# Kernel tuning notes

Measured on AMD Instinct MI355X. Metric: run time of the kernel, lower is better.

The kernel has to match this reference:

```python
import jax, jax.numpy as jnp
import numpy as np

MU = 0            # smeared direction (init arg dir)
IS_ODD = False    # init arg is_odd -> update the EVEN subset
DIMS = (24, 24, 24, 24)
N_PLAQ = 6
PI_2 = 0.6366197723675814  # 2/pi, as in scale_coeff


def setup_inputs() -> dict:
    key = jax.random.key(0)
    k1, k2, k3 = jax.random.split(key, 3)
    shape = (4,) + DIMS + (3, 3)  # [dir, T, Z, Y, X, 3, 3]
    x_re = jax.random.normal(k1, shape, jnp.float32)
    x_im = jax.random.normal(k2, shape, jnp.float32)
    coeff = jax.random.uniform(k3, (N_PLAQ,), jnp.float32)
    return {"x_re": x_re, "x_im": x_im, "coeff": coeff}


def _adj(m):
    return jnp.conj(jnp.swapaxes(m, -1, -2))


def _shift(a, nu, n):
    # lattice .shift(nu, n): value at site + n*nu_hat (periodic); lattice axes are the leading 4
    return jnp.roll(a, -n, axis=nu)


def _eo_filter(dims, is_odd, dtype):
    # evenodd_mask % 2; filter is 1 on the UPDATED subset (odd if is_odd else even)
    grids = jnp.meshgrid(*[jnp.arange(d) for d in dims], indexing='ij')
    parity = sum(grids) % 2
    mask = parity if is_odd else 1 - parity
    return mask.astype(dtype)[..., None, None]


def _matexp(Z, terms=12, squarings=4):
    # scaling-and-squaring Taylor (Horner) matrix exponential, batched over leading dims
    Z = Z * jnp.asarray(0.5 ** squarings, dtype=jnp.float32).astype(Z.dtype)
    eye = jnp.eye(Z.shape[-1], dtype=Z.dtype)
    E = eye
    for k in range(terms, 0, -1):
        E = eye + (Z @ E) / k
    for _ in range(squarings):
        E = E @ E
    return E


def reference(x_re, x_im, coeff):
    x = (x_re + 1j * x_im).astype(jnp.complex64)  # [4, T, Z, Y, X, 3, 3]
    filt = _eo_filter(DIMS, IS_ODD, jnp.complex64)
    # filter_fixed_update: mask mu-links; staples built from fixed-subset x[mu]
    xmu_fix = x[MU] * (1.0 - filt)
    xupd = x[MU] * filt
    # scale_coeff(coeff, 0.75) = (2/pi)*0.75*atan(coeff)
    c = (PI_2 * 0.75) * jnp.arctan(coeff)
    cc = c.astype(jnp.complex64)
    # plaquette staples (n_plaq = 6 loops)
    loops = []
    for nu in range(4):
        if nu == MU:
            continue
        Umu = _shift(xmu_fix, nu, 1)      # x[mu].shift(nu, 1)
        Unu = _shift(x[nu], MU, 1)        # x[nu].shift(mu, 1)
        R = Umu @ _adj(Unu)
        stf = x[nu] @ R                   # forward staple
        L = _adj(x[nu]) @ xmu_fix
        stu = L @ Unu
        loops.append(stf)
        loops.append(_shift(stu, nu, -1)) # backward staple
    f = loops[0] * cc[0]
    for i in range(1, N_PLAQ):
        f = f + loops[i] * cc[i]
    f = f / N_PLAQ
    # stout update on the updated subset: Z = projectTangent(f @ xupd^dag); U' = exp(Z) @ U
    M = f @ _adj(xupd)
    A = 0.5 * (M - _adj(M))               # anti-hermitian part
    tr = jnp.trace(A, axis1=-2, axis2=-1)
    Zt = A - (tr / 3.0)[..., None, None] * jnp.eye(3, dtype=A.dtype)  # traceless
    E = _matexp(Zt)
    ymu = E @ xupd + xmu_fix              # combine updated and fixed subsets
    y = x.at[MU].set(ymu)
    # return real/imag stacked so output is real-valued: [4, T, Z, Y, X, 3, 3, 2]
    return jnp.stack((jnp.real(y), jnp.imag(y)), axis=-1)
```

## Files before the change

### kernel.cpp

```cpp
#include <hip/hip_runtime.h>
#include <cstdint>

#define LT 24
#define NSITE (LT*LT*LT*LT)

struct C3 { float re[9]; float im[9]; };

__device__ __forceinline__ void load9(float* d, const float* __restrict__ p) {
    float4 a, b;
    __builtin_memcpy(&a, p,     16);
    __builtin_memcpy(&b, p + 4, 16);
    d[0]=a.x; d[1]=a.y; d[2]=a.z; d[3]=a.w;
    d[4]=b.x; d[5]=b.y; d[6]=b.z; d[7]=b.w;
    d[8]=p[8];
}

__device__ __forceinline__ void loadM(C3& m, const float* __restrict__ re,
                                      const float* __restrict__ im, int off) {
    load9(m.re, re + off);
    load9(m.im, im + off);
}

__device__ __forceinline__ void storeM(float2* __restrict__ out, int cbase, const C3& m) {
    float4 v;
    v.x=m.re[0]; v.y=m.im[0]; v.z=m.re[1]; v.w=m.im[1];
    __builtin_memcpy(out + cbase,     &v, 16);
    v.x=m.re[2]; v.y=m.im[2]; v.z=m.re[3]; v.w=m.im[3];
    __builtin_memcpy(out + cbase + 2, &v, 16);
    v.x=m.re[4]; v.y=m.im[4]; v.z=m.re[5]; v.w=m.im[5];
    __builtin_memcpy(out + cbase + 4, &v, 16);
    v.x=m.re[6]; v.y=m.im[6]; v.z=m.re[7]; v.w=m.im[7];
    __builtin_memcpy(out + cbase + 6, &v, 16);
    float2 w; w.x=m.re[8]; w.y=m.im[8];
    out[cbase + 8] = w;
}

__device__ __forceinline__ void mmul(C3& o, const C3& a, const C3& b) {
#pragma unroll
    for (int r = 0; r < 3; ++r) {
#pragma unroll
        for (int c = 0; c < 3; ++c) {
            float sr = 0.f, si = 0.f;
#pragma unroll
            for (int k = 0; k < 3; ++k) {
                float ar = a.re[r*3+k], ai = a.im[r*3+k];
                float br = b.re[k*3+c], bi = b.im[k*3+c];
                sr += ar*br - ai*bi;
                si += ar*bi + ai*br;
            }
            o.re[r*3+c] = sr; o.im[r*3+c] = si;
        }
    }
}

__device__ __forceinline__ void mmul_acc(C3& f, const C3& a, const C3& b, float cr) {
#pragma unroll
    for (int r = 0; r < 3; ++r) {
#pragma unroll
        for (int c = 0; c < 3; ++c) {
            float sr = 0.f, si = 0.f;
#pragma unroll
            for (int k = 0; k < 3; ++k) {
                float ar = a.re[r*3+k], ai = a.im[r*3+k];
                float br = b.re[k*3+c], bi = b.im[k*3+c];
                sr += ar*br - ai*bi;
                si += ar*bi + ai*br;
            }
            f.re[r*3+c] += cr * sr; f.im[r*3+c] += cr * si;
        }
    }
}

__device__ __forceinline__ void mmul_adjB(C3& o, const C3& a, const C3& b) {
#pragma unroll
    for (int r = 0; r < 3; ++r) {
#pragma unroll
        for (int c = 0; c < 3; ++c) {
            float sr = 0.f, si = 0.f;
#pragma unroll
            for (int k = 0; k < 3; ++k) {
                float ar = a.re[r*3+k], ai = a.im[r*3+k];
                float br = b.re[c*3+k], bi = b.im[c*3+k];
                sr += ar*br + ai*bi;
                si += ai*br - ar*bi;
            }
            o.re[r*3+c] = sr; o.im[r*3+c] = si;
        }
    }
}

__device__ __forceinline__ void madjA_mul(C3& o, const C3& a, const C3& b) {
#pragma unroll
    for (int r = 0; r < 3; ++r) {
#pragma unroll
        for (int c = 0; c < 3; ++c) {
            float sr = 0.f, si = 0.f;
#pragma unroll
            for (int k = 0; k < 3; ++k) {
                float ar = a.re[k*3+r], ai = a.im[k*3+r];
                float br = b.re[k*3+c], bi = b.im[k*3+c];
                sr += ar*br + ai*bi;
                si += ar*bi - ai*br;
            }
            o.re[r*3+c] = sr; o.im[r*3+c] = si;
        }
    }
}

__device__ __forceinline__ int site_from_idx(int idx, int parity,
                                             int& t, int& z, int& y, int& x) {
    int xh = idx % 12;  int r = idx / 12;
    y = r % LT; r /= LT;
    z = r % LT; t = r / LT;
    x = 2 * xh + ((t + z + y + parity) & 1);
    return ((t * LT + z) * LT + y) * LT + x;
}

__global__ __launch_bounds__(256)
void stout_fused(const float* __restrict__ xre, const float* __restrict__ xim,
                 const float* __restrict__ coeff, float2* __restrict__ out) {
    const int tau = threadIdx.x;
    const bool heavy = (tau < 128);
    const int idx = blockIdx.x * 128 + (heavy ? tau : tau - 128);

    if (!heavy) {
        int t, z, y, x;
        const int s = site_from_idx(idx, 1, t, z, y, x);
        C3 m;
#pragma unroll
        for (int d = 0; d < 4; ++d) {
            const int off = (d * NSITE + s) * 9;
            loadM(m, xre, xim, off);
            storeM(out, off, m);
        }
        return;
    }

    int t, z, y, x;
    const int s = site_from_idx(idx, 0, t, z, y, x);

    float c[6];
#pragma unroll
    for (int i = 0; i < 6; ++i)
        c[i] = 0.07957747154594768f * atanf(coeff[i]);

    int tp = (t + 1 < LT) ? t + 1 : 0;
    int zp = (z + 1 < LT) ? z + 1 : 0;  int zm = (z > 0) ? z - 1 : LT - 1;
    int yp = (y + 1 < LT) ? y + 1 : 0;  int ym = (y > 0) ? y - 1 : LT - 1;
    int xp = (x + 1 < LT) ? x + 1 : 0;  int xm = (x > 0) ? x - 1 : LT - 1;

    const int stt = ((tp * LT + z) * LT + y) * LT + x;
    const int spv[3]  = { ((t  * LT + zp) * LT + y ) * LT + x,
                          ((t  * LT + z ) * LT + yp) * LT + x,
                          ((t  * LT + z ) * LT + y ) * LT + xp };
    const int smv[3]  = { ((t  * LT + zm) * LT + y ) * LT + x,
                          ((t  * LT + z ) * LT + ym) * LT + x,
                          ((t  * LT + z ) * LT + y ) * LT + xm };
    const int smtv[3] = { ((tp * LT + zm) * LT + y ) * LT + x,
                          ((tp * LT + z ) * LT + ym) * LT + x,
                          ((tp * LT + z ) * LT + y ) * LT + xm };

    C3 f;
#pragma unroll
    for (int j = 0; j < 9; ++j) { f.re[j] = 0.f; f.im[j] = 0.f; }

    C3 A, B, Cm, tmp;
#pragma unroll
    for (int i = 0; i < 3; ++i) {
        const int d = i + 1;
        loadM(A, xre, xim, (d * NSITE + s) * 9);
        storeM(out, (d * NSITE + s) * 9, A);
        loadM(B,  xre, xim, (     spv[i])        * 9);
        loadM(Cm, xre, xim, (d * NSITE + stt)    * 9);
        mmul_adjB(tmp, B, Cm);
        mmul_acc(f, A, tmp, c[2 * i]);
        loadM(A,  xre, xim, (d * NSITE + smv[i]) * 9);
        loadM(B,  xre, xim, (     smv[i])        * 9);
        loadM(Cm, xre, xim, (d * NSITE + smtv[i])* 9);
        madjA_mul(tmp, A, B);
        mmul_acc(f, tmp, Cm, c[2 * i + 1]);
    }

    C3 U;
    loadM(U, xre, xim, s * 9);

    C3 Mm;
    mmul_adjB(Mm, f, U);
    C3 Zt;
#pragma unroll
    for (int r = 0; r < 3; ++r) {
#pragma unroll
        for (int cq = 0; cq < 3; ++cq) {
            Zt.re[r*3+cq] = 0.5f * (Mm.re[r*3+cq] - Mm.re[cq*3+r]);
            Zt.im[r*3+cq] = 0.5f * (Mm.im[r*3+cq] + Mm.im[cq*3+r]);
        }
    }
    float trIm = (Zt.im[0] + Zt.im[4] + Zt.im[8]) / 3.0f;
    Zt.im[0] -= trIm; Zt.im[4] -= trIm; Zt.im[8] -= trIm;

#pragma unroll
    for (int j = 0; j < 9; ++j) { Zt.re[j] *= 0.0625f; Zt.im[j] *= 0.0625f; }

    C3 E;
#pragma unroll
    for (int j = 0; j < 9; ++j) { E.re[j] = 0.f; E.im[j] = 0.f; }
    E.re[0] = 1.f; E.re[4] = 1.f; E.re[8] = 1.f;

    C3 Tm;
#pragma unroll
    for (int k = 12; k >= 1; --k) {
        mmul(Tm, Zt, E);
        const float invk = 1.0f / (float)k;
#pragma unroll
        for (int j = 0; j < 9; ++j) {
            E.re[j] = Tm.re[j] * invk;
            E.im[j] = Tm.im[j] * invk;
        }
        E.re[0] += 1.f; E.re[4] += 1.f; E.re[8] += 1.f;
    }
#pragma unroll
    for (int q = 0; q < 4; ++q) {
        mmul(Tm, E, E);
        E = Tm;
    }

    C3 Y;
    mmul(Y, E, U);
    storeM(out, s * 9, Y);
}

extern "C" void kernel_launch(void* const* d_in, const int* in_sizes, int n_in,
                              void* d_out, int out_size, void* d_ws, size_t ws_size,
                              hipStream_t stream) {
    const float* xre   = (const float*)d_in[0];
    const float* xim   = (const float*)d_in[1];
    const float* coeff = (const float*)d_in[2];

    const int nblocks = (NSITE / 2) / 128;
    stout_fused<<<nblocks, 256, 0, stream>>>(xre, xim, coeff, (float2*)d_out);
}
```

Measured before the change: 247.7 us.

## Split passthrough copy into coalesced interleave kernel and separate stout update

```diff
diff --git a/kernel.cpp b/kernel.cpp
--- a/kernel.cpp
+++ b/kernel.cpp
@@ -3,6 +3,7 @@
 
 #define LT 24
 #define NSITE (LT*LT*LT*LT)
+#define NCOMPLEX (4*NSITE*9)
 
 struct C3 { float re[9]; float im[9]; };
 
@@ -117,24 +118,27 @@
 }
 
 __global__ __launch_bounds__(256)
-void stout_fused(const float* __restrict__ xre, const float* __restrict__ xim,
-                 const float* __restrict__ coeff, float2* __restrict__ out) {
-    const int tau = threadIdx.x;
-    const bool heavy = (tau < 128);
-    const int idx = blockIdx.x * 128 + (heavy ? tau : tau - 128);
-
-    if (!heavy) {
-        int t, z, y, x;
-        const int s = site_from_idx(idx, 1, t, z, y, x);
-        C3 m;
-#pragma unroll
-        for (int d = 0; d < 4; ++d) {
-            const int off = (d * NSITE + s) * 9;
-            loadM(m, xre, xim, off);
-            storeM(out, off, m);
-        }
-        return;
-    }
+void interleave_copy(const float* __restrict__ xre, const float* __restrict__ xim,
+                     float4* __restrict__ out) {
+    const float4* __restrict__ re4 = (const float4*)xre;
+    const float4* __restrict__ im4 = (const float4*)xim;
+    const int nquad  = NCOMPLEX / 4;
+    const int stride = gridDim.x * blockDim.x;
+    for (int q = blockIdx.x * blockDim.x + threadIdx.x; q < nquad; q += stride) {
+        float4 r = re4[q];
+        float4 i = im4[q];
+        float4 o0, o1;
+        o0.x = r.x; o0.y = i.x; o0.z = r.y; o0.w = i.y;
+        o1.x = r.z; o1.y = i.z; o1.z = r.w; o1.w = i.w;
+        out[2*q]     = o0;
+        out[2*q + 1] = o1;
+    }
+}
+
+__global__ __launch_bounds__(256)
+void stout_update(const float* __restrict__ xre, const float* __restrict__ xim,
+                  const float* __restrict__ coeff, float2* __restrict__ out) {
+    const int idx = blockIdx.x * 256 + threadIdx.x;
 
     int t, z, y, x;
     const int s = site_from_idx(idx, 0, t, z, y, x);
@@ -169,7 +173,6 @@
     for (int i = 0; i < 3; ++i) {
         const int d = i + 1;
         loadM(A, xre, xim, (d * NSITE + s) * 9);
-        storeM(out, (d * NSITE + s) * 9, A);
         loadM(B,  xre, xim, (     spv[i])        * 9);
         loadM(Cm, xre, xim, (d * NSITE + stt)    * 9);
         mmul_adjB(tmp, B, Cm);
@@ -236,6 +239,8 @@
     const float* xim   = (const float*)d_in[1];
     const float* coeff = (const float*)d_in[2];
 
-    const int nblocks = (NSITE / 2) / 128;
-    stout_fused<<<nblocks, 256, 0, stream>>>(xre, xim, coeff, (float2*)d_out);
-}
+    interleave_copy<<<2048, 256, 0, stream>>>(xre, xim, (float4*)d_out);
+
+    const int nblocks = (NSITE / 2) / 256;
+    stout_update<<<nblocks, 256, 0, stream>>>(xre, xim, coeff, (float2*)d_out);
+}
```

New measurement: 241.2 us. 1.03x faster.

## Split work into heavy update, odd-copy, and vectorized bulk-copy block roles

Applied to the files above, without the earlier changes.

```diff
diff --git a/kernel.cpp b/kernel.cpp
--- a/kernel.cpp
+++ b/kernel.cpp
@@ -3,6 +3,16 @@
 
 #define LT 24
 #define NSITE (LT*LT*LT*LT)
+#define HALF  (NSITE/2)
+#define NCOMPLEX (4*NSITE*9)
+
+#define NB_UPD 648
+#define NB_ODD 648
+#define NB_CPY 2048
+#define CPY_Q0 (NSITE*9/4)
+#define CPY_NQ (3*NSITE*9/4)
+
+typedef float vf4 __attribute__((ext_vector_type(4)));
 
 struct C3 { float re[9]; float im[9]; };
 
@@ -116,25 +126,39 @@
     return ((t * LT + z) * LT + y) * LT + x;
 }
 
-__global__ __launch_bounds__(256)
-void stout_fused(const float* __restrict__ xre, const float* __restrict__ xim,
-                 const float* __restrict__ coeff, float2* __restrict__ out) {
-    const int tau = threadIdx.x;
-    const bool heavy = (tau < 128);
-    const int idx = blockIdx.x * 128 + (heavy ? tau : tau - 128);
-
-    if (!heavy) {
+__global__ __launch_bounds__(256, 4)
+void stout_all(const float* __restrict__ xre, const float* __restrict__ xim,
+               const float* __restrict__ coeff, float2* __restrict__ out) {
+    const int bid = blockIdx.x;
+
+    if (bid >= NB_UPD + NB_ODD) {
+        const vf4* __restrict__ re4 = (const vf4*)xre;
+        const vf4* __restrict__ im4 = (const vf4*)xim;
+        vf4* __restrict__ o4 = (vf4*)out;
+        const int tid = (bid - (NB_UPD + NB_ODD)) * 256 + threadIdx.x;
+        for (int j = tid; j < CPY_NQ; j += NB_CPY * 256) {
+            const int q = CPY_Q0 + j;
+            vf4 r = re4[q];
+            vf4 i = im4[q];
+            vf4 o0 = { r.x, i.x, r.y, i.y };
+            vf4 o1 = { r.z, i.z, r.w, i.w };
+            __builtin_nontemporal_store(o0, o4 + 2*q);
+            __builtin_nontemporal_store(o1, o4 + 2*q + 1);
+        }
+        return;
+    }
+
+    if (bid >= NB_UPD) {
+        const int idx = (bid - NB_UPD) * 256 + threadIdx.x;
         int t, z, y, x;
         const int s = site_from_idx(idx, 1, t, z, y, x);
         C3 m;
-#pragma unroll
-        for (int d = 0; d < 4; ++d) {
-            const int off = (d * NSITE + s) * 9;
-            loadM(m, xre, xim, off);
-            storeM(out, off, m);
-        }
+        loadM(m, xre, xim, s * 9);
+        storeM(out, s * 9, m);
         return;
     }
+
+    const int idx = bid * 256 + threadIdx.x;
 
     int t, z, y, x;
     const int s = site_from_idx(idx, 0, t, z, y, x);
@@ -169,15 +193,14 @@
     for (int i = 0; i < 3; ++i) {
         const int d = i + 1;
         loadM(A, xre, xim, (d * NSITE + s) * 9);
-        storeM(out, (d * NSITE + s) * 9, A);
         loadM(B,  xre, xim, (     spv[i])        * 9);
         loadM(Cm, xre, xim, (d * NSITE + stt)    * 9);
         mmul_adjB(tmp, B, Cm);
         mmul_acc(f, A, tmp, c[2 * i]);
         loadM(A,  xre, xim, (d * NSITE + smv[i]) * 9);
         loadM(B,  xre, xim, (     smv[i])        * 9);
+        madjA_mul(tmp, A, B);
         loadM(Cm, xre, xim, (d * NSITE + smtv[i])* 9);
-        madjA_mul(tmp, A, B);
         mmul_acc(f, tmp, Cm, c[2 * i + 1]);
     }
 
@@ -236,6 +259,6 @@
     const float* xim   = (const float*)d_in[1];
     const float* coeff = (const float*)d_in[2];
 
-    const int nblocks = (NSITE / 2) / 128;
-    stout_fused<<<nblocks, 256, 0, stream>>>(xre, xim, coeff, (float2*)d_out);
-}
+    const int nblocks = NB_UPD + NB_ODD + NB_CPY;
+    stout_all<<<nblocks, 256, 0, stream>>>(xre, xim, coeff, (float2*)d_out);
+}
```

After: 369.3 us. +49.1%, slower.

## Split work into heavy, odd-site, and bulk-copy block roles with contiguous vector copy

Applied to the files above, without the earlier changes.

```diff
diff --git a/kernel.cpp b/kernel.cpp
--- a/kernel.cpp
+++ b/kernel.cpp
@@ -3,6 +3,16 @@
 
 #define LT 24
 #define NSITE (LT*LT*LT*LT)
+#define HALF  (NSITE/2)
+#define NCOMPLEX (4*NSITE*9)
+
+#define NB_TOT 3240
+#define NB_CPY 1944
+#define CPY_THREADS (NB_CPY*256)
+#define Q0D (NSITE*9/2)
+#define NQD (3*NSITE*9/2)
+
+typedef float vf4 __attribute__((ext_vector_type(4)));
 
 struct C3 { float re[9]; float im[9]; };
 
@@ -117,24 +127,39 @@
 }
 
 __global__ __launch_bounds__(256)
-void stout_fused(const float* __restrict__ xre, const float* __restrict__ xim,
-                 const float* __restrict__ coeff, float2* __restrict__ out) {
-    const int tau = threadIdx.x;
-    const bool heavy = (tau < 128);
-    const int idx = blockIdx.x * 128 + (heavy ? tau : tau - 128);
-
-    if (!heavy) {
+void stout_all(const float* __restrict__ xre, const float* __restrict__ xim,
+               const float* __restrict__ coeff, float2* __restrict__ out) {
+    const int bid  = blockIdx.x;
+    const int role = bid % 5;
+    const int sub  = bid / 5;
+
+    if (role >= 2) {
+        const float2* __restrict__ re2 = (const float2*)xre;
+        const float2* __restrict__ im2 = (const float2*)xim;
+        vf4* __restrict__ o4 = (vf4*)out;
+        const int cid = sub * 3 + (role - 2);
+        int q = Q0D + cid * 256 + threadIdx.x;
+#pragma unroll
+        for (int it = 0; it < 9; ++it, q += CPY_THREADS) {
+            float2 r = re2[q];
+            float2 i = im2[q];
+            vf4 o = { r.x, i.x, r.y, i.y };
+            __builtin_nontemporal_store(o, o4 + q);
+        }
+        return;
+    }
+
+    if (role == 1) {
+        const int idx = sub * 256 + threadIdx.x;
         int t, z, y, x;
         const int s = site_from_idx(idx, 1, t, z, y, x);
         C3 m;
-#pragma unroll
-        for (int d = 0; d < 4; ++d) {
-            const int off = (d * NSITE + s) * 9;
-            loadM(m, xre, xim, off);
-            storeM(out, off, m);
-        }
+        loadM(m, xre, xim, s * 9);
+        storeM(out, s * 9, m);
         return;
     }
+
+    const int idx = sub * 256 + threadIdx.x;
 
     int t, z, y, x;
     const int s = site_from_idx(idx, 0, t, z, y, x);
@@ -169,15 +194,14 @@
     for (int i = 0; i < 3; ++i) {
         const int d = i + 1;
         loadM(A, xre, xim, (d * NSITE + s) * 9);
-        storeM(out, (d * NSITE + s) * 9, A);
         loadM(B,  xre, xim, (     spv[i])        * 9);
         loadM(Cm, xre, xim, (d * NSITE + stt)    * 9);
         mmul_adjB(tmp, B, Cm);
         mmul_acc(f, A, tmp, c[2 * i]);
         loadM(A,  xre, xim, (d * NSITE + smv[i]) * 9);
         loadM(B,  xre, xim, (     smv[i])        * 9);
+        madjA_mul(tmp, A, B);
         loadM(Cm, xre, xim, (d * NSITE + smtv[i])* 9);
-        madjA_mul(tmp, A, B);
         mmul_acc(f, tmp, Cm, c[2 * i + 1]);
     }
 
@@ -236,6 +260,5 @@
     const float* xim   = (const float*)d_in[1];
     const float* coeff = (const float*)d_in[2];
 
-    const int nblocks = (NSITE / 2) / 128;
-    stout_fused<<<nblocks, 256, 0, stream>>>(xre, xim, coeff, (float2*)d_out);
-}
+    stout_all<<<NB_TOT, 256, 0, stream>>>(xre, xim, coeff, (float2*)d_out);
+}
```

New measurement: 216.0 us. -12.8%, faster.
